# Kernel tuning notes

Measured on AMD Instinct MI355X. Metric: run time of the kernel, lower is better.

The kernel has to match this reference:

```python
import jax, jax.numpy as jnp
import numpy as np

NUM_HEADS = 32
HEAD_DIM = 128
ROPE_THETA = 10000.0


def _rope_tables(seq_len, head_dim, theta):
    inv_freq = 1.0 / (theta ** (jnp.arange(0, head_dim, 2, dtype=jnp.float32) / head_dim))
    pos = jnp.arange(seq_len, dtype=jnp.float32)
    freqs = pos[:, None] * inv_freq[None, :]            # [S, hd/2]
    emb = jnp.concatenate([freqs, freqs], axis=-1)      # [S, hd]
    return jnp.cos(emb), jnp.sin(emb)


def _rotate_half(x):
    x1, x2 = jnp.split(x, 2, axis=-1)
    return jnp.concatenate([-x2, x1], axis=-1)


def _apply_rope(x, cos, sin):
    # x: [B, S, H, D]; cos/sin: [S, D] -> unsqueeze_dim=2 broadcasting
    c = cos[None, :, None, :]
    s = sin[None, :, None, :]
    return x * c + _rotate_half(x) * s


def setup_inputs() -> dict:
    key = jax.random.key(0)
    ks = jax.random.split(key, 6)
    hidden = 4096
    B, S = 2, 4096  # global sequence = world_size * local_seq (4 * 1024)
    hidden_states = jax.random.normal(ks[0], (B, S, hidden), dtype=jnp.float32)
    # original uses torch.rand (uniform); scaled by 0.02 for numerical sanity
    q_proj = jax.random.uniform(ks[1], (hidden, hidden), dtype=jnp.float32) * 0.02
    k_proj = jax.random.uniform(ks[2], (hidden, hidden), dtype=jnp.float32) * 0.02
    v_proj = jax.random.uniform(ks[3], (hidden, hidden), dtype=jnp.float32) * 0.02
    o_proj = jax.random.uniform(ks[4], (hidden, hidden), dtype=jnp.float32) * 0.02
    return {"hidden_states": hidden_states, "q_proj": q_proj, "k_proj": k_proj,
            "v_proj": v_proj, "o_proj": o_proj, "world_size": 4}


def _ring_attention(hidden_states, q_proj, k_proj, v_proj, o_proj, world_size):
    B, S, H = hidden_states.shape
    s_local = S // world_size
    nh, hd = NUM_HEADS, HEAD_DIM
    scale = 1.0 / np.sqrt(hd).astype(np.float32)

    # rank 0 holds the first sequence shard as its local hidden states
    hs_local = hidden_states[:, :s_local]
    q = (hs_local @ q_proj.T).reshape(B, s_local, nh, hd)
    k = (hidden_states @ k_proj.T).reshape(B, S, nh, hd)
    v = (hidden_states @ v_proj.T).reshape(B, S, nh, hd)

    cos, sin = _rope_tables(S, hd, ROPE_THETA)
    q = _apply_rope(q, cos[:s_local], sin[:s_local])   # rank0 positions 0..s_local-1
    k = _apply_rope(k, cos, sin)                       # global positions per shard

    # split into per-rank KV blocks; rank 0 receives blocks W-1, W-2, ..., 0
    k_blocks = k.reshape(B, world_size, s_local, nh, hd).transpose(1, 0, 2, 3, 4)[::-1]
    v_blocks = v.reshape(B, world_size, s_local, nh, hd).transpose(1, 0, 2, 3, 4)[::-1]

    def step(carry, kv):
        attn, max_lse, denom, lse_full = carry
        k_blk, v_blk = kv
        # memory_efficient_attention_partial: non-causal partial attention + lse
        s = jnp.einsum('bqhd,bkhd->bhqk', q, k_blk) * scale
        m = jnp.max(s, axis=-1)                          # [B,H,q]
        p = jnp.exp(s - m[..., None])
        l = jnp.sum(p, axis=-1)
        lse = (m + jnp.log(l)).transpose(0, 2, 1)        # [B,q,H]
        out = jnp.einsum('bhqk,bkhd->bqhd', p / l[..., None], v_blk)
        # online-softmax merge across ring steps
        new_max = jnp.maximum(max_lse, lse)
        old_adj = jnp.exp(max_lse - new_max)[..., None]
        new_adj = jnp.exp(lse - new_max)[..., None]
        denom = old_adj * denom + new_adj
        attn = old_adj * attn + new_adj * out
        lse_full = new_max + jnp.log(jnp.exp(lse_full - new_max) + jnp.exp(lse - new_max))
        return (attn, new_max, denom, lse_full), None

    init = (jnp.zeros((B, s_local, nh, hd), jnp.float32),
            jnp.full((B, s_local, nh), -jnp.inf, jnp.float32),
            jnp.zeros((B, s_local, nh, 1), jnp.float32),
            jnp.full((B, s_local, nh), -jnp.inf, jnp.float32))
    (attn, _, denom, _), _ = jax.lax.scan(step, init, (k_blocks, v_blocks))

    attn = attn / denom
    attn = attn.astype(jnp.float16).astype(jnp.float32)  # .half() in source
    attn = attn.reshape(B, s_local, nh * hd)
    return attn @ o_proj.T


def reference(hidden_states, q_proj, k_proj, v_proj, o_proj, world_size):
    return _ring_attention(hidden_states, q_proj, k_proj, v_proj, o_proj, world_size)
```

## Files before the change

### kernel.cpp

```cpp
#include <hip/hip_runtime.h>


using bf16x8 = __attribute__((ext_vector_type(8))) short;
using f32x4  = __attribute__((ext_vector_type(4))) float;

__device__ inline unsigned short f32_to_bf16_bits(float f) {
  unsigned int u = __float_as_uint(f);
  u += 0x7FFFu + ((u >> 16) & 1u);
  return (unsigned short)(u >> 16);
}
__device__ inline float bf16_bits_to_f32(unsigned short h) {
  return __uint_as_float(((unsigned int)h) << 16);
}

__device__ __forceinline__ void load_lds16(const unsigned short* g, unsigned short* l) {
  __builtin_amdgcn_global_load_lds(
      (const __attribute__((address_space(1))) void*)g,
      (__attribute__((address_space(3))) void*)l, 16, 0, 0);
}

__global__ void cast_f32_bf16(const float* __restrict__ in,
                              unsigned short* __restrict__ out, long n4) {
  long i = (long)blockIdx.x * blockDim.x + threadIdx.x;
  long stride = (long)gridDim.x * blockDim.x;
  for (; i < n4; i += stride) {
    float4 v = reinterpret_cast<const float4*>(in)[i];
    ushort4 o;
    o.x = f32_to_bf16_bits(v.x);
    o.y = f32_to_bf16_bits(v.y);
    o.z = f32_to_bf16_bits(v.z);
    o.w = f32_to_bf16_bits(v.w);
    reinterpret_cast<ushort4*>(out)[i] = o;
  }
}

__global__ void rope_tables(float* __restrict__ cos_t, float* __restrict__ sin_t) {
  int idx = blockIdx.x * 256 + threadIdx.x;
  if (idx >= 4096 * 64) return;
  int p = idx >> 6, i = idx & 63;
  float inv = __expf(-(float)i * (9.210340371976184f / 64.0f));
  float f = (float)p * inv;
  cos_t[idx] = cosf(f);
  sin_t[idx] = sinf(f);
}

__global__ void rope_apply_v(unsigned short* __restrict__ buf,
                             const float4* __restrict__ cos4,
                             const float4* __restrict__ sin4,
                             long nchunks, int pos_mask, float gain) {
  long idx = (long)blockIdx.x * 256 + threadIdx.x;
  if (idx >= nchunks) return;
  long tok = idx >> 8;
  int rem = (int)(idx & 255);
  int head = rem >> 3, c = rem & 7;
  int pos = (int)(tok & (long)pos_mask);
  float4 ct0 = cos4[pos * 16 + c * 2];
  float4 ct1 = cos4[pos * 16 + c * 2 + 1];
  float4 st0 = sin4[pos * 16 + c * 2];
  float4 st1 = sin4[pos * 16 + c * 2 + 1];
  float cs[8] = {ct0.x, ct0.y, ct0.z, ct0.w, ct1.x, ct1.y, ct1.z, ct1.w};
  float sn[8] = {st0.x, st0.y, st0.z, st0.w, st1.x, st1.y, st1.z, st1.w};
  long base = tok * 4096 + head * 128 + c * 8;
  bf16x8 x1 = *reinterpret_cast<const bf16x8*>(buf + base);
  bf16x8 x2 = *reinterpret_cast<const bf16x8*>(buf + base + 64);
  bf16x8 o1, o2;
#pragma unroll
  for (int j = 0; j < 8; j++) {
    float a = bf16_bits_to_f32((unsigned short)x1[j]);
    float b = bf16_bits_to_f32((unsigned short)x2[j]);
    o1[j] = (short)f32_to_bf16_bits((a * cs[j] - b * sn[j]) * gain);
    o2[j] = (short)f32_to_bf16_bits((b * cs[j] + a * sn[j]) * gain);
  }
  *reinterpret_cast<bf16x8*>(buf + base) = o1;
  *reinterpret_cast<bf16x8*>(buf + base + 64) = o2;
}

__device__ inline void storeC(float* p, float v) { *p = v; }
__device__ inline void storeC(unsigned short* p, float v) { *p = f32_to_bf16_bits(v); }

template <typename OUT_T>
__global__ __launch_bounds__(256) void gemm_bt(const unsigned short* __restrict__ A,
                                               const unsigned short* __restrict__ B,
                                               OUT_T* __restrict__ C,
                                               long Astride_z, long Cstride_z, int N) {
  __shared__ unsigned short As[128 * 32];
  __shared__ unsigned short Bs[128 * 32];
  const int tid = threadIdx.x;
  const int bn = blockIdx.x, bm = blockIdx.y, bz = blockIdx.z;
  const unsigned short* Ab = A + (long)bz * Astride_z + (long)bm * 128 * 4096;
  const unsigned short* Bb = B + (long)bn * 128 * 4096;
  OUT_T* Cb = C + (long)bz * Cstride_z + (long)bm * 128 * N + (long)bn * 128;

  const int lane = tid & 63;
  const int w = tid >> 6;
  const int wr = (w >> 1) * 64, wc = (w & 1) * 64;
  const int fr = lane & 15, fg = lane >> 4;

  f32x4 acc[4][4] = {};

  const int c0 = tid, c1 = tid + 256;
  const int rA0 = c0 >> 2, kc0 = c0 & 3;
  const int rA1 = c1 >> 2, kc1 = c1 & 3;

  for (int k0 = 0; k0 < 4096; k0 += 32) {
    load_lds16(Ab + (long)rA0 * 4096 + k0 + kc0 * 8, As + c0 * 8);
    load_lds16(Ab + (long)rA1 * 4096 + k0 + kc1 * 8, As + c1 * 8);
    load_lds16(Bb + (long)rA0 * 4096 + k0 + kc0 * 8, Bs + c0 * 8);
    load_lds16(Bb + (long)rA1 * 4096 + k0 + kc1 * 8, Bs + c1 * 8);
    __syncthreads();
    bf16x8 af[4], bfv[4];
#pragma unroll
    for (int m = 0; m < 4; m++)
      af[m] = *reinterpret_cast<const bf16x8*>(As + (wr + m * 16 + fr) * 32 + fg * 8);
#pragma unroll
    for (int n = 0; n < 4; n++)
      bfv[n] = *reinterpret_cast<const bf16x8*>(Bs + (wc + n * 16 + fr) * 32 + fg * 8);
#pragma unroll
    for (int m = 0; m < 4; m++)
#pragma unroll
      for (int n = 0; n < 4; n++)
        acc[m][n] = __builtin_amdgcn_mfma_f32_16x16x32_bf16(af[m], bfv[n], acc[m][n], 0, 0, 0);
    __syncthreads();
  }
#pragma unroll
  for (int m = 0; m < 4; m++)
#pragma unroll
    for (int n = 0; n < 4; n++)
#pragma unroll
      for (int r = 0; r < 4; r++) {
        int row = wr + m * 16 + fg * 4 + r;
        int col = wc + n * 16 + fr;
        storeC(Cb + (long)row * N + col, acc[m][n][r]);
      }
}

#define STG2(Gb, Lb, h, kc)                                                    \
  load_lds16((Gb) + (long)((h) * 128 + srow) * 4096 + sslot * 8 + (kc),        \
             (Lb) + tid * 8);                                                  \
  load_lds16((Gb) + (long)((h) * 128 + 64 + srow) * 4096 + sslot * 8 + (kc),   \
             (Lb) + 4096 + tid * 8);

#define MFMAQ(MH, NH)                                                          \
  _Pragma("unroll") for (int mi = 0; mi < 4; ++mi)                             \
    _Pragma("unroll") for (int ni = 0; ni < 2; ++ni)                           \
      _Pragma("unroll") for (int kk = 0; kk < 2; ++kk)                         \
        acc[(MH) * 4 + mi][(NH) * 2 + ni] =                                    \
            __builtin_amdgcn_mfma_f32_16x16x32_bf16(                           \
                a[mi][kk], b[(NH) * 2 + ni][kk],                               \
                acc[(MH) * 4 + mi][(NH) * 2 + ni], 0, 0, 0);

#define TILE(P, KC, MODE)                                                      \
  {                                                                            \
    const unsigned short* Ar = lds + wm * 16384 + (P) * 8192;                  \
    const unsigned short* Br =                                                 \
        lds + 32768 + (wn >> 1) * 16384 + (P) * 8192 + (wn & 1) * 4096;        \
    _Pragma("unroll") for (int mf = 0; mf < 4; ++mf) {                         \
      a[mf][0] = *reinterpret_cast<const bf16x8*>(Ar + mf * 1024 + ao0);       \
      a[mf][1] = *reinterpret_cast<const bf16x8*>(Ar + mf * 1024 + ao1);       \
    }                                                                          \
    _Pragma("unroll") for (int nf = 0; nf < 2; ++nf) {                         \
      b[nf][0] = *reinterpret_cast<const bf16x8*>(Br + nf * 1024 + ao0);       \
      b[nf][1] = *reinterpret_cast<const bf16x8*>(Br + nf * 1024 + ao1);       \
    }                                                                          \
    __builtin_amdgcn_s_setprio(1);                                             \
    MFMAQ(0, 0);                                                               \
    __builtin_amdgcn_s_setprio(0);                                             \
    _Pragma("unroll") for (int nf = 2; nf < 4; ++nf) {                         \
      b[nf][0] = *reinterpret_cast<const bf16x8*>(Br + nf * 1024 + ao0);       \
      b[nf][1] = *reinterpret_cast<const bf16x8*>(Br + nf * 1024 + ao1);       \
    }                                                                          \
    __builtin_amdgcn_s_setprio(1);                                             \
    MFMAQ(0, 1);                                                               \
    __builtin_amdgcn_s_setprio(0);                                             \
    asm volatile("s_waitcnt lgkmcnt(0)" ::: "memory");                         \
    asm volatile("s_barrier" ::: "memory");            \
    if ((MODE) == 0) {                                                         \
      STG2(Bg, lds + 32768 + (P) * 8192, 0, KC);                               \
      STG2(Bg, lds + 49152 + (P) * 8192, 1, KC);                               \
    }                                                                          \
    _Pragma("unroll") for (int mf = 0; mf < 4; ++mf) {                         \
      a[mf][0] = *reinterpret_cast<const bf16x8*>(Ar + (4 + mf) * 1024 + ao0); \
      a[mf][1] = *reinterpret_cast<const bf16x8*>(Ar + (4 + mf) * 1024 + ao1); \
    }                                                                          \
    __builtin_amdgcn_s_setprio(1);                                             \
    MFMAQ(1, 0);                                                               \
    __builtin_amdgcn_s_setprio(0);                                             \
    asm volatile("s_waitcnt lgkmcnt(0)" ::: "memory");                         \
    asm volatile("s_barrier" ::: "memory");            \
    if ((MODE) == 0) {                                                         \
      STG2(Ag, lds + (P) * 8192, 0, KC);                                       \
      STG2(Ag, lds + 16384 + (P) * 8192, 1, KC);                               \
    }                                                                          \
    __builtin_amdgcn_s_setprio(1);                                             \
    MFMAQ(1, 1);                                                               \
    __builtin_amdgcn_s_setprio(0);                                             \
    if ((MODE) == 0) asm volatile("s_waitcnt vmcnt(8)" ::: "memory");          \
    if ((MODE) == 1) asm volatile("s_waitcnt vmcnt(0)" ::: "memory");          \
    asm volatile("s_barrier" ::: "memory");       \
  }

template <typename OUT_T>
__global__ __launch_bounds__(512, 2) void gemm256(const unsigned short* __restrict__ A,
                                                  const unsigned short* __restrict__ B,
                                                  OUT_T* __restrict__ C,
                                                  long Astride_z, long Cstride_z, int N) {
  __shared__ unsigned short lds[65536];
  const int tid = threadIdx.x;
  const int bn = blockIdx.x, bm = blockIdx.y, bz = blockIdx.z;
  const unsigned short* Ag = A + (long)bz * Astride_z + (long)bm * 256 * 4096;
  const unsigned short* Bg = B + (long)bn * 256 * 4096;

  const int w = tid >> 6, lane = tid & 63;
  const int wm = w >> 2, wn = w & 3;
  const int fr = lane & 15, fg = lane >> 4;
  const int ao0 = fr * 64 + ((fg ^ (fr & 7)) * 8);
  const int ao1 = fr * 64 + (((4 + fg) ^ (fr & 7)) * 8);
  const int srow = tid >> 3;
  const int sslot = (tid & 7) ^ (srow & 7);

  f32x4 acc[8][4] = {};
  bf16x8 a[4][2], b[4][2];

  STG2(Ag, lds + 0, 0, 0);     STG2(Ag, lds + 16384, 1, 0);
  STG2(Bg, lds + 32768, 0, 0); STG2(Bg, lds + 49152, 1, 0);
  STG2(Ag, lds + 8192, 0, 64);  STG2(Ag, lds + 24576, 1, 64);
  STG2(Bg, lds + 40960, 0, 64); STG2(Bg, lds + 57344, 1, 64);
  asm volatile("s_waitcnt vmcnt(8)" ::: "memory");
  asm volatile("s_barrier" ::: "memory");

  for (int ti = 0; ti < 31; ++ti) {
    TILE(0, (2 * ti + 2) * 64, 0);
    TILE(1, (2 * ti + 3) * 64, 0);
  }
  TILE(0, 0, 1);
  TILE(1, 0, 2);

  OUT_T* Cb = C + (long)bz * Cstride_z + ((long)bm * 256) * N + bn * 256;
#pragma unroll
  for (int mf = 0; mf < 8; ++mf)
#pragma unroll
    for (int nf = 0; nf < 4; ++nf)
#pragma unroll
      for (int rr = 0; rr < 4; ++rr) {
        int row = wm * 128 + mf * 16 + fg * 4 + rr;
        int col = wn * 64 + nf * 16 + fr;
        storeC(Cb + (long)row * N + col, acc[mf][nf][rr]);
      }
}

#define AT_STAGE(P, kv)                                                        \
  _Pragma("unroll") for (int i = 0; i < 4; i++) {                              \
    int c = tid + 256 * i;                                                     \
    int key = c >> 4, s0 = c & 15;                                             \
    int Lg = s0 ^ (key & 15);                                                  \
    load_lds16(kbase + (long)((kv) + key) * 4096 + Lg * 8, &Ks[P][c * 8]);     \
  }                                                                            \
  _Pragma("unroll") for (int i = 0; i < 4; i++) {                              \
    int c = tid + 256 * i;                                                     \
    int f0 = c >> 3, s0 = c & 7;                                               \
    int Lg = s0 ^ (f0 & 7);                                                    \
    load_lds16(vbase + (long)f0 * 8192 + (kv) + Lg * 8, &Vl[P][c * 8]);        \
  }

__global__ __launch_bounds__(256) void attn_fwd(const unsigned short* __restrict__ qb,
                                                const unsigned short* __restrict__ kb,
                                                const unsigned short* __restrict__ vT,
                                                unsigned short* __restrict__ ob) {
  __shared__ unsigned short Ks[2][64 * 128];
  __shared__ unsigned short Vl[2][128 * 64];
  __shared__ unsigned short Ps[4][16 * 72];

  const int qt = blockIdx.x, h = blockIdx.y, b = blockIdx.z;
  const int tid = threadIdx.x, w = tid >> 6, lane = tid & 63;
  const int fr = lane & 15, fg = lane >> 4;

  const unsigned short* kbase = kb + (long)b * 4096 * 4096 + h * 128;
  const unsigned short* vbase = vT + (long)h * 128 * 8192 + (long)b * 4096;

  bf16x8 qf[4];
  {
    const unsigned short* qptr =
        qb + ((long)b * 1024 + qt * 64 + w * 16 + fr) * 4096 + h * 128 + fg * 8;
#pragma unroll
    for (int c = 0; c < 4; c++) qf[c] = *reinterpret_cast<const bf16x8*>(qptr + c * 32);
  }

  f32x4 outa[8] = {};
  float m_run[4], l_run[4];
#pragma unroll
  for (int r = 0; r < 4; r++) { m_run[r] = -1e30f; l_run[r] = 0.0f; }

  AT_STAGE(0, 0);
  asm volatile("s_waitcnt vmcnt(0)" ::: "memory");
  asm volatile("s_barrier" ::: "memory");

  for (int t = 0; t < 64; ++t) {
    const int cur = t & 1;
    if (t < 63) { AT_STAGE(cur ^ 1, (t + 1) * 64); }

    f32x4 sacc[4];
#pragma unroll
    for (int ks = 0; ks < 4; ks++) {
      f32x4 aq = {0.f, 0.f, 0.f, 0.f};
#pragma unroll
      for (int cc = 0; cc < 4; cc++) {
        bf16x8 kf = *reinterpret_cast<const bf16x8*>(
            &Ks[cur][(ks * 16 + fr) * 128 + (((cc * 4 + fg) ^ fr) & 15) * 8]);
        aq = __builtin_amdgcn_mfma_f32_16x16x32_bf16(qf[cc], kf, aq, 0, 0, 0);
      }
      sacc[ks] = aq;
    }

    float mx4[4];
#pragma unroll
    for (int r = 0; r < 4; r++) {
      float mx = fmaxf(fmaxf(sacc[0][r], sacc[1][r]), fmaxf(sacc[2][r], sacc[3][r]));
      mx = fmaxf(mx, __shfl_xor(mx, 1));
      mx = fmaxf(mx, __shfl_xor(mx, 2));
      mx = fmaxf(mx, __shfl_xor(mx, 4));
      mx = fmaxf(mx, __shfl_xor(mx, 8));
      mx4[r] = mx;
    }
    int need = 0;
#pragma unroll
    for (int r = 0; r < 4; r++) need |= (mx4[r] > m_run[r] + 11.5f) ? 1 : 0;
    if (__any(need)) {
#pragma unroll
      for (int r = 0; r < 4; r++) {
        float mnew = fmaxf(m_run[r], mx4[r]);
        float ef = exp2f(m_run[r] - mnew);
        l_run[r] *= ef;
        m_run[r] = mnew;
#pragma unroll
        for (int ds = 0; ds < 8; ds++) outa[ds][r] *= ef;
      }
    }
#pragma unroll
    for (int r = 0; r < 4; r++) {
      float sum = 0.f;
#pragma unroll
      for (int ks = 0; ks < 4; ks++) {
        float pv = exp2f(sacc[ks][r] - m_run[r]);
        Ps[w][(fg * 4 + r) * 72 + ks * 16 + fr] = f32_to_bf16_bits(pv);
        sum += pv;
      }
      l_run[r] += sum;
    }

#pragma unroll
    for (int c2 = 0; c2 < 2; c2++) {
      bf16x8 pf = *reinterpret_cast<const bf16x8*>(&Ps[w][fr * 72 + c2 * 32 + fg * 8]);
#pragma unroll
      for (int ds = 0; ds < 8; ds++) {
        int feat = ds * 16 + fr;
        int pch = ((c2 * 4 + fg) ^ (feat & 7)) & 7;
        bf16x8 vf = *reinterpret_cast<const bf16x8*>(&Vl[cur][feat * 64 + pch * 8]);
        outa[ds] = __builtin_amdgcn_mfma_f32_16x16x32_bf16(pf, vf, outa[ds], 0, 0, 0);
      }
    }

    if (t < 63) {
      asm volatile("s_waitcnt lgkmcnt(0)" ::: "memory");
      asm volatile("s_waitcnt vmcnt(0)" ::: "memory");
      asm volatile("s_barrier" ::: "memory");
    }
  }

#pragma unroll
  for (int r = 0; r < 4; r++) {
    float l = l_run[r];
    l += __shfl_xor(l, 1);
    l += __shfl_xor(l, 2);
    l += __shfl_xor(l, 4);
    l += __shfl_xor(l, 8);
    float inv = 1.0f / l;
    unsigned short* op =
        ob + ((long)b * 1024 + qt * 64 + w * 16 + fg * 4 + r) * 4096 + h * 128;
#pragma unroll
    for (int ds = 0; ds < 8; ds++) op[ds * 16 + fr] = f32_to_bf16_bits(outa[ds][r] * inv);
  }
}

extern "C" void kernel_launch(void* const* d_in, const int* in_sizes, int n_in,
                              void* d_out, int out_size, void* d_ws, size_t ws_size,
                              hipStream_t stream) {
  const float* hs = (const float*)d_in[0];
  const float* wq = (const float*)d_in[1];
  const float* wk = (const float*)d_in[2];
  const float* wv = (const float*)d_in[3];
  const float* wo = (const float*)d_in[4];
  float* out = (float*)d_out;

  const long hsN = 2L * 4096 * 4096;
  const long wN  = 4096L * 4096;

  unsigned short* hs_b = (unsigned short*)d_ws;
  unsigned short* wq_b = hs_b + hsN;
  unsigned short* wk_b = wq_b + wN;
  unsigned short* wv_b = wk_b + wN;
  unsigned short* wo_b = wv_b + wN;
  unsigned short* q_b  = wo_b + wN;
  unsigned short* k_b  = q_b + 2048L * 4096;
  unsigned short* vT_b = k_b + 8192L * 4096;
  unsigned short* at_b = vT_b + 8192L * 4096;
  float* cos_t = (float*)(at_b + 2048L * 4096);
  float* sin_t = cos_t + 4096 * 64;

  cast_f32_bf16<<<dim3(4096), dim3(256), 0, stream>>>(hs, hs_b, hsN / 4);
  cast_f32_bf16<<<dim3(2048), dim3(256), 0, stream>>>(wq, wq_b, wN / 4);
  cast_f32_bf16<<<dim3(2048), dim3(256), 0, stream>>>(wk, wk_b, wN / 4);
  cast_f32_bf16<<<dim3(2048), dim3(256), 0, stream>>>(wv, wv_b, wN / 4);
  cast_f32_bf16<<<dim3(2048), dim3(256), 0, stream>>>(wo, wo_b, wN / 4);

  rope_tables<<<dim3(1024), dim3(256), 0, stream>>>(cos_t, sin_t);

  gemm_bt<unsigned short><<<dim3(32, 8, 2), dim3(256), 0, stream>>>(
      hs_b, wq_b, q_b, 4096L * 4096, 1024L * 4096, 4096);
  gemm256<unsigned short><<<dim3(16, 16, 2), dim3(512), 0, stream>>>(
      hs_b, wk_b, k_b, 4096L * 4096, 4096L * 4096, 4096);
  gemm256<unsigned short><<<dim3(32, 16, 1), dim3(512), 0, stream>>>(
      wv_b, hs_b, vT_b, 0L, 0L, 8192);

  const float qgain = 0.08838834764831845f * 1.4426950408889634f;
  rope_apply_v<<<dim3(2048), dim3(256), 0, stream>>>(
      q_b, (const float4*)cos_t, (const float4*)sin_t, 2048L * 256, 1023, qgain);
  rope_apply_v<<<dim3(8192), dim3(256), 0, stream>>>(
      k_b, (const float4*)cos_t, (const float4*)sin_t, 8192L * 256, 4095, 1.0f);

  attn_fwd<<<dim3(16, 32, 2), dim3(256), 0, stream>>>(q_b, k_b, vT_b, at_b);

  gemm_bt<float><<<dim3(32, 16, 1), dim3(256), 0, stream>>>(
      at_b, wo_b, out, 0L, 0L, 4096);
}
```

Before: 1.078 ms.

## Batch input casts into one launch and tune attention softmax scheduling

The five separate f32-to-bf16 cast launches become one grid-stride kernel that writes into the contiguous workspace, which removes per-launch overhead. In the attention loop, the cross-lane max reduction now runs only when some lane's local max exceeds the running max by the threshold, so most iterations skip the shuffles. MFMA sections are wrapped in s_setprio to favour matrix issue, and the two waitcnts are merged into one. The batched cast adds a per-element division and source selection, and the lazy max keeps the running max stale within the bounded threshold.

Measured after the change: 1.022 ms. 5.2% less time.

```diff
diff --git a/kernel.cpp b/kernel.cpp
--- a/kernel.cpp
+++ b/kernel.cpp
@@ -19,12 +19,28 @@
       (__attribute__((address_space(3))) void*)l, 16, 0, 0);
 }
 
-__global__ void cast_f32_bf16(const float* __restrict__ in,
-                              unsigned short* __restrict__ out, long n4) {
+__global__ void cast_f32_bf16_batched(const float* __restrict__ hs,
+                                      const float* __restrict__ w0,
+                                      const float* __restrict__ w1,
+                                      const float* __restrict__ w2,
+                                      const float* __restrict__ w3,
+                                      unsigned short* __restrict__ out) {
+  const long hs4 = 2L * 4096 * 4096 / 4;
+  const long w4  = 4096L * 4096 / 4;
   long i = (long)blockIdx.x * blockDim.x + threadIdx.x;
   long stride = (long)gridDim.x * blockDim.x;
-  for (; i < n4; i += stride) {
-    float4 v = reinterpret_cast<const float4*>(in)[i];
+  const long total = hs4 + 4 * w4;
+  for (; i < total; i += stride) {
+    const float* src;
+    long j = i;
+    if (j < hs4) { src = hs; }
+    else {
+      j -= hs4;
+      long wi = j / w4;
+      j -= wi * w4;
+      src = (wi == 0) ? w0 : (wi == 1) ? w1 : (wi == 2) ? w2 : w3;
+    }
+    float4 v = reinterpret_cast<const float4*>(src)[j];
     ushort4 o;
     o.x = f32_to_bf16_bits(v.x);
     o.y = f32_to_bf16_bits(v.y);
@@ -299,6 +315,7 @@
     if (t < 63) { AT_STAGE(cur ^ 1, (t + 1) * 64); }
 
     f32x4 sacc[4];
+    __builtin_amdgcn_s_setprio(1);
 #pragma unroll
     for (int ks = 0; ks < 4; ks++) {
       f32x4 aq = {0.f, 0.f, 0.f, 0.f};
@@ -310,24 +327,24 @@
       }
       sacc[ks] = aq;
     }
-
-    float mx4[4];
+    __builtin_amdgcn_s_setprio(0);
+
+    float mxl[4];
+    int need = 0;
 #pragma unroll
     for (int r = 0; r < 4; r++) {
-      float mx = fmaxf(fmaxf(sacc[0][r], sacc[1][r]), fmaxf(sacc[2][r], sacc[3][r]));
-      mx = fmaxf(mx, __shfl_xor(mx, 1));
-      mx = fmaxf(mx, __shfl_xor(mx, 2));
-      mx = fmaxf(mx, __shfl_xor(mx, 4));
-      mx = fmaxf(mx, __shfl_xor(mx, 8));
-      mx4[r] = mx;
-    }
-    int need = 0;
-#pragma unroll
-    for (int r = 0; r < 4; r++) need |= (mx4[r] > m_run[r] + 11.5f) ? 1 : 0;
+      mxl[r] = fmaxf(fmaxf(sacc[0][r], sacc[1][r]), fmaxf(sacc[2][r], sacc[3][r]));
+      need |= (mxl[r] > m_run[r] + 11.5f) ? 1 : 0;
+    }
     if (__any(need)) {
 #pragma unroll
       for (int r = 0; r < 4; r++) {
-        float mnew = fmaxf(m_run[r], mx4[r]);
+        float mx = mxl[r];
+        mx = fmaxf(mx, __shfl_xor(mx, 1));
+        mx = fmaxf(mx, __shfl_xor(mx, 2));
+        mx = fmaxf(mx, __shfl_xor(mx, 4));
+        mx = fmaxf(mx, __shfl_xor(mx, 8));
+        float mnew = fmaxf(m_run[r], mx);
         float ef = exp2f(m_run[r] - mnew);
         l_run[r] *= ef;
         m_run[r] = mnew;
@@ -347,6 +364,7 @@
       l_run[r] += sum;
     }
 
+    __builtin_amdgcn_s_setprio(1);
 #pragma unroll
     for (int c2 = 0; c2 < 2; c2++) {
       bf16x8 pf = *reinterpret_cast<const bf16x8*>(&Ps[w][fr * 72 + c2 * 32 + fg * 8]);
@@ -358,10 +376,10 @@
         outa[ds] = __builtin_amdgcn_mfma_f32_16x16x32_bf16(pf, vf, outa[ds], 0, 0, 0);
       }
     }
+    __builtin_amdgcn_s_setprio(0);
 
     if (t < 63) {
-      asm volatile("s_waitcnt lgkmcnt(0)" ::: "memory");
-      asm volatile("s_waitcnt vmcnt(0)" ::: "memory");
+      asm volatile("s_waitcnt vmcnt(0) lgkmcnt(0)" ::: "memory");
       asm volatile("s_barrier" ::: "memory");
     }
   }
@@ -406,11 +424,8 @@
   float* cos_t = (float*)(at_b + 2048L * 4096);
   float* sin_t = cos_t + 4096 * 64;
 
-  cast_f32_bf16<<<dim3(4096), dim3(256), 0, stream>>>(hs, hs_b, hsN / 4);
-  cast_f32_bf16<<<dim3(2048), dim3(256), 0, stream>>>(wq, wq_b, wN / 4);
-  cast_f32_bf16<<<dim3(2048), dim3(256), 0, stream>>>(wk, wk_b, wN / 4);
-  cast_f32_bf16<<<dim3(2048), dim3(256), 0, stream>>>(wv, wv_b, wN / 4);
-  cast_f32_bf16<<<dim3(2048), dim3(256), 0, stream>>>(wo, wo_b, wN / 4);
+  cast_f32_bf16_batched<<<dim3(8192), dim3(256), 0, stream>>>(
+      hs, wq, wk, wv, wo, hs_b);
 
   rope_tables<<<dim3(1024), dim3(256), 0, stream>>>(cos_t, sin_t);
 
```
